# Optimization experiments

Measured on AMD Instinct MI355X. Metric: run time of the kernel, lower is better.

The kernel has to match this reference:

```python
import jax, jax.numpy as jnp
import numpy as np

# Wrapped Conv2D config (channels_last): input 32x32x32 -> output 32x32x64, 3x3 'same', stride 1
H, W, C_IN, C_OUT = 32, 32, 32, 64


def _propagate(w, b, kernel, bias):
    # w: [B, H*W*C_OUT, n_out], b: [B, n_out]
    B, _, n_out = w.shape
    # transpose(0,2,1) + reshape to [B, n_out, H, W, C_OUT]
    wt = jnp.transpose(w, (0, 2, 1)).reshape(B, n_out, H, W, C_OUT)
    # bias-sum reduction: sum over (h, w, c) of w * bias[c], added to b
    b_new = jnp.einsum('bnhwc,c->bn', wt, bias) + b
    # Batched transposed conv over all n_out slices at once (replaces K.rnn loop)
    z = wt.reshape(B * n_out, H, W, C_OUT)
    w_in = jax.lax.conv_transpose(
        z, kernel, strides=(1, 1), padding='SAME',
        dimension_numbers=('NHWC', 'HWIO', 'NHWC'), transpose_kernel=True)
    # -> [B*n_out, H, W, C_IN]; flatten and transpose back to [B, n_in, n_out]
    w_new = jnp.transpose(w_in.reshape(B, n_out, H * W * C_IN), (0, 2, 1))
    return w_new, b_new


def setup_inputs() -> dict:
    key = jax.random.key(0)
    ks = jax.random.split(key, 6)
    B, n_out = 8, 32
    n_flat = H * W * C_OUT
    return {
        'w_out_u': jax.random.normal(ks[0], (B, n_flat, n_out), jnp.float32),
        'b_out_u': jax.random.normal(ks[1], (B, n_out), jnp.float32),
        'w_out_l': jax.random.normal(ks[2], (B, n_flat, n_out), jnp.float32),
        'b_out_l': jax.random.normal(ks[3], (B, n_out), jnp.float32),
        'kernel': jax.random.normal(ks[4], (3, 3, C_IN, C_OUT), jnp.float32) * 0.1,
        'bias': jax.random.normal(ks[5], (C_OUT,), jnp.float32) * 0.1,
    }


def reference(w_out_u, b_out_u, w_out_l, b_out_l, kernel, bias):
    w_u, b_u = _propagate(w_out_u, b_out_u, kernel, bias)
    w_l, b_l = _propagate(w_out_l, b_out_l, kernel, bias)
    return (w_u, b_u, w_l, b_l)
```

## Files before the change

### kernel.cpp

```cpp
#include <hip/hip_runtime.h>
#include <hip/hip_bf16.h>

#define H  32
#define W  32
#define CI 32
#define CO 64
#define NB 8
#define NOUT 32

#define WU_OFF 0
#define BU_OFF (NB * H * W * CI * NOUT)
#define WL_OFF (BU_OFF + NB * NOUT)
#define BL_OFF (WL_OFF + NB * H * W * CI * NOUT)

#define KF_UINT4 2304
#define BP_OFF_BYTES 36864

typedef __bf16 bf16x8 __attribute__((ext_vector_type(8)));
typedef float  f32x4  __attribute__((ext_vector_type(4)));

__device__ __forceinline__ unsigned int pack_bf16(float lo, float hi) {
    unsigned int ulo = __float_as_uint(lo) + 0x8000u;
    unsigned int uhi = __float_as_uint(hi) + 0x8000u;
    return (uhi & 0xffff0000u) | (ulo >> 16);
}

__global__ void prep_kernel(const float* __restrict__ K,
                            unsigned int* __restrict__ kws,
                            float* __restrict__ bp) {
    int bx = blockIdx.x, t = threadIdx.x;
    if (bx < 9) {
        int g    = bx * 256 + t;
        int tap  = g >> 8;
        int r    = g & 255;
        int i    = r >> 3;
        int og   = r & 7;
        int c    = og >> 2;
        int quad = og & 3;
        int ih   = i >> 4;
        int lane = quad * 16 + (i & 15);
        int dst  = ((tap * 4 + c * 2 + ih) * 64 + lane) * 4;
        const float4* src = (const float4*)(K + (size_t)g * 8);
        float4 f0 = src[0];
        float4 f1 = src[1];
        kws[dst + 0] = pack_bf16(f0.x, f0.y);
        kws[dst + 1] = pack_bf16(f0.z, f0.w);
        kws[dst + 2] = pack_bf16(f1.x, f1.y);
        kws[dst + 3] = pack_bf16(f1.z, f1.w);
    } else {
        bp[(bx - 9) * 256 + t] = 0.f;
    }
}

__global__ __launch_bounds__(512, 6)
void fused_conv_kernel(const float* __restrict__ in0,
                       const float* __restrict__ in1,
                       const uint4* __restrict__ kws,
                       const float* __restrict__ bias,
                       float* __restrict__ bp,
                       float* __restrict__ out0,
                       float* __restrict__ out1) {
    __shared__ uint4 stg[24 * 128];
    __shared__ float bias_s[CO];
    __shared__ float bsum[8][32];

    int t = threadIdx.x;
    if (t < CO) bias_s[t] = bias[t];

    int bx    = blockIdx.x;
    int x     = bx & 7;
    int q     = bx >> 3;
    int combo = x * 2 + (q >> 7);
    int inner = q & 127;
    int side  = combo >> 3;
    int b     = combo & 7;
    int h0    = (inner >> 3) * 2;
    int wq4   = inner & 7;

    const float* inp = (side ? in1 : in0) + (size_t)b * 1024 * 2048;
    const bf16x8* kfg = (const bf16x8*)kws;

    int unit = t >> 5;
    int ogp  = (t >> 3) & 3;
    int n4   = t & 7;
    int wave = t >> 6;
    int lane = t & 63;
    int n16  = lane & 15;
    int quad = lane >> 4;
    int wl   = wave & 3;
    int wh2  = wave >> 2;
    int h    = h0 + wh2;
    int w    = wq4 * 4 + wl;

    f32x4 acc[2][2] = {};
    float sb[4] = {0.f, 0.f, 0.f, 0.f};
    int rbase = quad * 32 + ((n16 ^ (n16 >> 2)) ^ quad);

    __syncthreads();

    for (int c = 0; c < 2; c++) {
#pragma unroll 1
        for (int s = 0; s < 2; s++) {
            int tile = s * 16 + unit;
            if (tile < 24) {
                int row = tile >= 18 ? 3 : (tile >= 12 ? 2 : (tile >= 6 ? 1 : 0));
                int col = tile - row * 6;
                int hi  = h0 - 1 + row;
                int wi  = wq4 * 4 - 1 + col;
                if (hi >= 0 && hi < H && wi >= 0 && wi < W) {
                    const float* p = inp + (size_t)(hi * W + wi) * 2048
                                   + c * 1024 + ogp * 256 + n4 * 4;
                    float v[8][4];
#pragma unroll
                    for (int j = 0; j < 8; j++) {
                        float4 f = *(const float4*)(p + j * 32);
                        v[j][0] = f.x; v[j][1] = f.y; v[j][2] = f.z; v[j][3] = f.w;
                    }
                    if ((row == 1 || row == 2) && col >= 1 && col <= 4) {
#pragma unroll
                        for (int j = 0; j < 8; j++) {
                            float bj = bias_s[c * 32 + ogp * 8 + j];
#pragma unroll
                            for (int k = 0; k < 4; k++)
                                sb[k] = fmaf(v[j][k], bj, sb[k]);
                        }
                    }
                    uint4* dst = &stg[tile * 128 + ogp * 32];
#pragma unroll
                    for (int k = 0; k < 4; k++) {
                        uint4 u;
                        u.x = pack_bf16(v[0][k], v[1][k]);
                        u.y = pack_bf16(v[2][k], v[3][k]);
                        u.z = pack_bf16(v[4][k], v[5][k]);
                        u.w = pack_bf16(v[6][k], v[7][k]);
                        int n = n4 * 4 + k;
                        dst[(n ^ (n >> 2)) ^ ogp] = u;
                    }
                }
            }
        }
        __syncthreads();
        __builtin_amdgcn_s_setprio(1);
#pragma unroll 1
        for (int kh = 0; kh < 3; kh++) {
            int hi = h + 1 - kh;
            if (hi < 0 || hi >= H) continue;
            int row = wh2 + 2 - kh;
#pragma unroll
            for (int kw = 0; kw < 3; kw++) {
                int wi = w + 1 - kw;
                if (wi < 0 || wi >= W) continue;
                int col = wl + 2 - kw;
                int tap = kh * 3 + kw;
                const uint4* Tp = &stg[(row * 6 + col) * 128];
                union { uint4 u; bf16x8 v; } b0, b1;
                b0.u = Tp[rbase];
                b1.u = Tp[rbase ^ 20];
                bf16x8 a0 = kfg[(tap * 4 + c * 2 + 0) * 64 + lane];
                bf16x8 a1 = kfg[(tap * 4 + c * 2 + 1) * 64 + lane];
                acc[0][0] = __builtin_amdgcn_mfma_f32_16x16x32_bf16(a0, b0.v, acc[0][0], 0, 0, 0);
                acc[0][1] = __builtin_amdgcn_mfma_f32_16x16x32_bf16(a0, b1.v, acc[0][1], 0, 0, 0);
                acc[1][0] = __builtin_amdgcn_mfma_f32_16x16x32_bf16(a1, b0.v, acc[1][0], 0, 0, 0);
                acc[1][1] = __builtin_amdgcn_mfma_f32_16x16x32_bf16(a1, b1.v, acc[1][1], 0, 0, 0);
            }
        }
        __builtin_amdgcn_s_setprio(0);
        if (c == 0) __syncthreads();
    }

#pragma unroll
    for (int off = 8; off <= 32; off <<= 1)
#pragma unroll
        for (int k = 0; k < 4; k++)
            sb[k] += __shfl_xor(sb[k], off, 64);
    if (lane < 8) {
#pragma unroll
        for (int k = 0; k < 4; k++)
            bsum[wave][lane * 4 + k] = sb[k];
    }
    __syncthreads();
    if (t < 32) {
        float s = 0.f;
#pragma unroll
        for (int wv = 0; wv < 8; wv++) s += bsum[wv][t];
        atomicAdd(&bp[side * 256 + b * 32 + t], s);
    }

    float* outp = (side ? out1 : out0) + (size_t)b * (H * W * CI * NOUT);
    float* wout = outp + (size_t)((h * W + w) * CI) * NOUT;
#pragma unroll
    for (int ih = 0; ih < 2; ih++)
#pragma unroll
        for (int nh = 0; nh < 2; nh++)
#pragma unroll
            for (int r = 0; r < 4; r++) {
                int i = ih * 16 + quad * 4 + r;
                int n = nh * 16 + n16;
                wout[i * NOUT + n] = acc[ih][nh][r];
            }
}

__global__ void bias_final32_kernel(const float* __restrict__ bp,
                                    const float* __restrict__ bu,
                                    const float* __restrict__ bl,
                                    float* __restrict__ out) {
    int sb = blockIdx.x;
    int t  = threadIdx.x;
    if (t >= NOUT) return;
    int side = sb >> 3, b = sb & 7;
    const float* bb = side ? bl : bu;
    out[(side ? BL_OFF : BU_OFF) + b * NOUT + t] =
        bb[b * NOUT + t] + bp[sb * 32 + t];
}

extern "C" void kernel_launch(void* const* d_in, const int* in_sizes, int n_in,
                              void* d_out, int out_size, void* d_ws, size_t ws_size,
                              hipStream_t stream) {
    const float* wu   = (const float*)d_in[0];
    const float* bu   = (const float*)d_in[1];
    const float* wl   = (const float*)d_in[2];
    const float* bl   = (const float*)d_in[3];
    const float* K    = (const float*)d_in[4];
    const float* bias = (const float*)d_in[5];
    float* out = (float*)d_out;
    unsigned int* kws = (unsigned int*)d_ws;
    float* bp = (float*)((char*)d_ws + BP_OFF_BYTES);

    prep_kernel<<<dim3(11), dim3(256), 0, stream>>>(K, kws, bp);
    fused_conv_kernel<<<dim3(2048), dim3(512), 0, stream>>>(
        wu, wl, (const uint4*)d_ws, bias, bp, out + WU_OFF, out + WL_OFF);
    bias_final32_kernel<<<dim3(16), dim3(64), 0, stream>>>(bp, bu, bl, out);
}
```

Before: 211.0 us.

## Prefetch second channel half into registers during first MFMA phase

Restructures the conv kernel so each thread issues global loads for both of its tiles up front, and issues the c=1 channel-half loads before running the c=0 MFMA phase. The aim is to overlap global-memory latency with matrix compute instead of serialising load then compute per half. Holding two 8x4 float buffers raises register pressure, so launch bounds drop from 6 to 4 waves-per-EU minimum. That lowers occupancy in exchange for software prefetch.

```diff
diff --git a/kernel.cpp b/kernel.cpp
--- a/kernel.cpp
+++ b/kernel.cpp
@@ -52,7 +52,72 @@
     }
 }
 
-__global__ __launch_bounds__(512, 6)
+__device__ __forceinline__ void load_tile(const float* p, int c, float v[8][4]) {
+#pragma unroll
+    for (int j = 0; j < 8; j++) {
+        float4 f = *(const float4*)(p + c * 1024 + j * 32);
+        v[j][0] = f.x; v[j][1] = f.y; v[j][2] = f.z; v[j][3] = f.w;
+    }
+}
+
+__device__ __forceinline__ void pack_write(const float v[8][4], int tile,
+                                           int ogp, int n4, uint4* stg) {
+    uint4* dst = &stg[tile * 128 + ogp * 32];
+#pragma unroll
+    for (int k = 0; k < 4; k++) {
+        uint4 u;
+        u.x = pack_bf16(v[0][k], v[1][k]);
+        u.y = pack_bf16(v[2][k], v[3][k]);
+        u.z = pack_bf16(v[4][k], v[5][k]);
+        u.w = pack_bf16(v[6][k], v[7][k]);
+        int n = n4 * 4 + k;
+        dst[(n ^ (n >> 2)) ^ ogp] = u;
+    }
+}
+
+__device__ __forceinline__ void bias_acc(const float v[8][4], const float* bias_s,
+                                         int c, int ogp, float sb[4]) {
+#pragma unroll
+    for (int j = 0; j < 8; j++) {
+        float bj = bias_s[c * 32 + ogp * 8 + j];
+#pragma unroll
+        for (int k = 0; k < 4; k++)
+            sb[k] = fmaf(v[j][k], bj, sb[k]);
+    }
+}
+
+__device__ __forceinline__ void mfma_phase(int c, int h, int w, int wh2, int wl,
+                                           int rbase, int lane,
+                                           const uint4* stg, const bf16x8* kfg,
+                                           f32x4 acc[2][2]) {
+    __builtin_amdgcn_s_setprio(1);
+#pragma unroll 1
+    for (int kh = 0; kh < 3; kh++) {
+        int hi = h + 1 - kh;
+        if (hi < 0 || hi >= H) continue;
+        int row = wh2 + 2 - kh;
+#pragma unroll
+        for (int kw = 0; kw < 3; kw++) {
+            int wi = w + 1 - kw;
+            if (wi < 0 || wi >= W) continue;
+            int col = wl + 2 - kw;
+            int tap = kh * 3 + kw;
+            const uint4* Tp = &stg[(row * 6 + col) * 128];
+            union { uint4 u; bf16x8 v; } b0, b1;
+            b0.u = Tp[rbase];
+            b1.u = Tp[rbase ^ 20];
+            bf16x8 a0 = kfg[(tap * 4 + c * 2 + 0) * 64 + lane];
+            bf16x8 a1 = kfg[(tap * 4 + c * 2 + 1) * 64 + lane];
+            acc[0][0] = __builtin_amdgcn_mfma_f32_16x16x32_bf16(a0, b0.v, acc[0][0], 0, 0, 0);
+            acc[0][1] = __builtin_amdgcn_mfma_f32_16x16x32_bf16(a0, b1.v, acc[0][1], 0, 0, 0);
+            acc[1][0] = __builtin_amdgcn_mfma_f32_16x16x32_bf16(a1, b0.v, acc[1][0], 0, 0, 0);
+            acc[1][1] = __builtin_amdgcn_mfma_f32_16x16x32_bf16(a1, b1.v, acc[1][1], 0, 0, 0);
+        }
+    }
+    __builtin_amdgcn_s_setprio(0);
+}
+
+__global__ __launch_bounds__(512, 4)
 void fused_conv_kernel(const float* __restrict__ in0,
                        const float* __restrict__ in1,
                        const uint4* __restrict__ kws,
@@ -92,81 +157,41 @@
     int h    = h0 + wh2;
     int w    = wq4 * 4 + wl;
 
+    int tA   = unit;
+    int rowA = tA >= 12 ? 2 : (tA >= 6 ? 1 : 0);
+    int colA = tA - rowA * 6;
+    int tB   = unit + 16;
+    int rowB = tB >= 18 ? 3 : 2;
+    int colB = tB - rowB * 6;
+    int hiA = h0 - 1 + rowA, wiA = wq4 * 4 - 1 + colA;
+    int hiB = h0 - 1 + rowB, wiB = wq4 * 4 - 1 + colB;
+    bool okA = (hiA >= 0 && hiA < H && wiA >= 0 && wiA < W);
+    bool okB = (tB < 24) && (hiB >= 0 && hiB < H && wiB >= 0 && wiB < W);
+    const float* pA = inp + (size_t)((hiA * W + wiA)) * 2048 + ogp * 256 + n4 * 4;
+    const float* pB = inp + (size_t)((hiB * W + wiB)) * 2048 + ogp * 256 + n4 * 4;
+    bool ownA = (rowA == 1 || rowA == 2) && colA >= 1 && colA <= 4;
+    bool ownB = (rowB == 2) && colB >= 1 && colB <= 4;
+
     f32x4 acc[2][2] = {};
     float sb[4] = {0.f, 0.f, 0.f, 0.f};
     int rbase = quad * 32 + ((n16 ^ (n16 >> 2)) ^ quad);
 
-    __syncthreads();
-
-    for (int c = 0; c < 2; c++) {
-#pragma unroll 1
-        for (int s = 0; s < 2; s++) {
-            int tile = s * 16 + unit;
-            if (tile < 24) {
-                int row = tile >= 18 ? 3 : (tile >= 12 ? 2 : (tile >= 6 ? 1 : 0));
-                int col = tile - row * 6;
-                int hi  = h0 - 1 + row;
-                int wi  = wq4 * 4 - 1 + col;
-                if (hi >= 0 && hi < H && wi >= 0 && wi < W) {
-                    const float* p = inp + (size_t)(hi * W + wi) * 2048
-                                   + c * 1024 + ogp * 256 + n4 * 4;
-                    float v[8][4];
-#pragma unroll
-                    for (int j = 0; j < 8; j++) {
-                        float4 f = *(const float4*)(p + j * 32);
-                        v[j][0] = f.x; v[j][1] = f.y; v[j][2] = f.z; v[j][3] = f.w;
-                    }
-                    if ((row == 1 || row == 2) && col >= 1 && col <= 4) {
-#pragma unroll
-                        for (int j = 0; j < 8; j++) {
-                            float bj = bias_s[c * 32 + ogp * 8 + j];
-#pragma unroll
-                            for (int k = 0; k < 4; k++)
-                                sb[k] = fmaf(v[j][k], bj, sb[k]);
-                        }
-                    }
-                    uint4* dst = &stg[tile * 128 + ogp * 32];
-#pragma unroll
-                    for (int k = 0; k < 4; k++) {
-                        uint4 u;
-                        u.x = pack_bf16(v[0][k], v[1][k]);
-                        u.y = pack_bf16(v[2][k], v[3][k]);
-                        u.z = pack_bf16(v[4][k], v[5][k]);
-                        u.w = pack_bf16(v[6][k], v[7][k]);
-                        int n = n4 * 4 + k;
-                        dst[(n ^ (n >> 2)) ^ ogp] = u;
-                    }
-                }
-            }
-        }
-        __syncthreads();
-        __builtin_amdgcn_s_setprio(1);
-#pragma unroll 1
-        for (int kh = 0; kh < 3; kh++) {
-            int hi = h + 1 - kh;
-            if (hi < 0 || hi >= H) continue;
-            int row = wh2 + 2 - kh;
-#pragma unroll
-            for (int kw = 0; kw < 3; kw++) {
-                int wi = w + 1 - kw;
-                if (wi < 0 || wi >= W) continue;
-                int col = wl + 2 - kw;
-                int tap = kh * 3 + kw;
-                const uint4* Tp = &stg[(row * 6 + col) * 128];
-                union { uint4 u; bf16x8 v; } b0, b1;
-                b0.u = Tp[rbase];
-                b1.u = Tp[rbase ^ 20];
-                bf16x8 a0 = kfg[(tap * 4 + c * 2 + 0) * 64 + lane];
-                bf16x8 a1 = kfg[(tap * 4 + c * 2 + 1) * 64 + lane];
-                acc[0][0] = __builtin_amdgcn_mfma_f32_16x16x32_bf16(a0, b0.v, acc[0][0], 0, 0, 0);
-                acc[0][1] = __builtin_amdgcn_mfma_f32_16x16x32_bf16(a0, b1.v, acc[0][1], 0, 0, 0);
-                acc[1][0] = __builtin_amdgcn_mfma_f32_16x16x32_bf16(a1, b0.v, acc[1][0], 0, 0, 0);
-                acc[1][1] = __builtin_amdgcn_mfma_f32_16x16x32_bf16(a1, b1.v, acc[1][1], 0, 0, 0);
-            }
-        }
-        __builtin_amdgcn_s_setprio(0);
-        if (c == 0) __syncthreads();
-    }
+    float vA[8][4], vB[8][4];
+
+    if (okA) load_tile(pA, 0, vA);
+    if (okB) load_tile(pB, 0, vB);
+    __syncthreads();
+    if (okA) { if (ownA) bias_acc(vA, bias_s, 0, ogp, sb); pack_write(vA, tA, ogp, n4, stg); }
+    if (okB) { if (ownB) bias_acc(vB, bias_s, 0, ogp, sb); pack_write(vB, tB, ogp, n4, stg); }
+    if (okA) load_tile(pA, 1, vA);
+    if (okB) load_tile(pB, 1, vB);
+    __syncthreads();
+    mfma_phase(0, h, w, wh2, wl, rbase, lane, stg, kfg, acc);
+    __syncthreads();
+    if (okA) { if (ownA) bias_acc(vA, bias_s, 1, ogp, sb); pack_write(vA, tA, ogp, n4, stg); }
+    if (okB) { if (ownB) bias_acc(vB, bias_s, 1, ogp, sb); pack_write(vB, tB, ogp, n4, stg); }
+    __syncthreads();
+    mfma_phase(1, h, w, wh2, wl, rbase, lane, stg, kfg, acc);
 
 #pragma unroll
     for (int off = 8; off <= 32; off <<= 1)
```

Measured after the change: 204.9 us. 1.03x faster.
